# Performance work log

Hardware: AMD Instinct MI355X
Metric: run time of the kernel (lower is better)

## Reference

```python
import jax, jax.numpy as jnp
import numpy as np

N = 100000      # nodes
E = 1600000     # edges
F_IN = 512      # num_node_features
HID = 128       # hidden_dim (GCN2Conv channels)
C = 64          # num_classes
L = 8           # n_layers
ALPHA = 0.1
THETA = 0.5


def setup_inputs() -> dict:
    key = jax.random.key(0)
    ks = jax.random.split(key, 7)
    x = jax.random.normal(ks[0], (N, F_IN), jnp.float32)
    edge_index = jax.random.randint(ks[1], (2, E), 0, N, dtype=jnp.int64)
    # fcs[0]: Linear(F_IN, HID); stored as [in, out] so forward is x @ w + b
    w_in = jax.random.normal(ks[2], (F_IN, HID), jnp.float32) / np.sqrt(F_IN)
    b_in = jnp.zeros((HID,), jnp.float32)
    # one shared [H, H] weight per GCN2Conv layer (shared_weights=True)
    conv_w = jax.random.normal(ks[3], (L, HID, HID), jnp.float32) / np.sqrt(HID)
    # fcs[-1]: Linear(HID, C)
    w_out = jax.random.normal(ks[4], (HID, C), jnp.float32) / np.sqrt(HID)
    b_out = jnp.zeros((C,), jnp.float32)
    return dict(x=x, edge_index=edge_index, w_in=w_in, b_in=b_in,
                conv_w=conv_w, w_out=w_out, b_out=b_out)


def _gcn_norm(edge_index, num_nodes):
    # PyG gcn_norm with add_self_loops=True, edge_weight=1
    loops = jnp.arange(num_nodes, dtype=edge_index.dtype)
    src = jnp.concatenate([edge_index[0], loops])
    dst = jnp.concatenate([edge_index[1], loops])
    deg = jax.ops.segment_sum(jnp.ones_like(dst, jnp.float32), dst,
                              num_segments=num_nodes)
    dinv = jnp.where(deg > 0, jax.lax.rsqrt(jnp.maximum(deg, 1e-12)), 0.0)
    norm = dinv[src] * dinv[dst]  # [E + N]
    return src, dst, norm


def reference(x, edge_index, w_in, b_in, conv_w, w_out, b_out):
    src, dst, norm = _gcn_norm(edge_index, N)
    h = x @ w_in + b_in          # fcs[0]; [N, HID]
    h0 = h                       # initial residual
    for l in range(L):
        beta = float(np.log(THETA / (l + 1) + 1.0))
        # sparse neighbor aggregation: out[i] = sum_e norm[e] * h[src[e]]
        agg = jax.ops.segment_sum(h[src] * norm[:, None], dst, num_segments=N)
        s = (1.0 - ALPHA) * agg + ALPHA * h0           # initial residual mix
        h = jax.nn.elu((1.0 - beta) * s + beta * (s @ conv_w[l]))  # identity mapping
        # dropout omitted (eval mode / training=False)
    logits = h @ w_out + b_out   # fcs[-1]
    return jax.nn.log_softmax(logits, axis=-1)
```

## Files before the change

kernel.cpp:

```cpp
#include <hip/hip_runtime.h>
#include <math.h>

#define N_NODES 100000
#define N_EDGES 1600000
#define F_IN    512
#define HID     128
#define NCLS    64
#define NLAYERS 8
#define NT      (N_NODES / 16)
#define NSCANB  ((N_NODES + 255) / 256)

typedef __attribute__((ext_vector_type(8))) short short8;
typedef __attribute__((ext_vector_type(4))) float float4v;

__device__ inline unsigned short f2bf(float f) {
    unsigned int u = __float_as_uint(f);
    unsigned int r = u + 0x7fffu + ((u >> 16) & 1u);
    return (unsigned short)(r >> 16);
}
__device__ inline float bf2f(unsigned short h) {
    return __uint_as_float(((unsigned int)h) << 16);
}
__device__ inline uint4 pack8(const unsigned short* v) {
    uint4 u;
    u.x = (unsigned)v[0] | ((unsigned)v[1] << 16);
    u.y = (unsigned)v[2] | ((unsigned)v[3] << 16);
    u.z = (unsigned)v[4] | ((unsigned)v[5] << 16);
    u.w = (unsigned)v[6] | ((unsigned)v[7] << 16);
    return u;
}
__device__ inline void bf8_fma(float* a, uint4 u, float v) {
    a[0] += v * __uint_as_float(u.x << 16);
    a[1] += v * __uint_as_float(u.x & 0xffff0000u);
    a[2] += v * __uint_as_float(u.y << 16);
    a[3] += v * __uint_as_float(u.y & 0xffff0000u);
    a[4] += v * __uint_as_float(u.z << 16);
    a[5] += v * __uint_as_float(u.z & 0xffff0000u);
    a[6] += v * __uint_as_float(u.w << 16);
    a[7] += v * __uint_as_float(u.w & 0xffff0000u);
}
__device__ inline void split_into(short8& ahi, short8& alo, int j, float f) {
    unsigned short h = f2bf(f);
    ahi[j] = (short)h;
    alo[j] = (short)f2bf(f - bf2f(h));
}


__global__ __launch_bounds__(256) void cnt_init(int* __restrict__ cnt) {
    int i = blockIdx.x * 256 + threadIdx.x;
    if (i < N_NODES) cnt[i] = 0;
}
__global__ __launch_bounds__(256) void cnt_count(const int* __restrict__ dst,
                                                 int* __restrict__ cnt) {
    int e = blockIdx.x * 256 + threadIdx.x;
    if (e < N_EDGES) atomicAdd(&cnt[dst[e]], 1);
}
__global__ __launch_bounds__(256) void make_dinv(const int* __restrict__ cnt,
                                                 float* __restrict__ dinv) {
    int i = blockIdx.x * 256 + threadIdx.x;
    if (i < N_NODES) dinv[i] = rsqrtf((float)(cnt[i] + 1));
}
__global__ __launch_bounds__(256) void scan_block(const int* __restrict__ cnt,
                                                  int* __restrict__ partial,
                                                  int* __restrict__ bsum) {
    __shared__ int tmp[256];
    int t = threadIdx.x, i = blockIdx.x * 256 + t;
    int v = (i < N_NODES) ? cnt[i] : 0;
    tmp[t] = v;
    __syncthreads();
#pragma unroll
    for (int off = 1; off < 256; off <<= 1) {
        int add = (t >= off) ? tmp[t - off] : 0;
        __syncthreads();
        tmp[t] += add;
        __syncthreads();
    }
    if (i < N_NODES) partial[i] = tmp[t];
    if (t == 255) bsum[blockIdx.x] = tmp[255];
}
__global__ void scan_bsum(int* __restrict__ bsum) {
    if (threadIdx.x == 0 && blockIdx.x == 0) {
        int acc = 0;
        for (int i = 0; i < NSCANB; i++) { int v = bsum[i]; bsum[i] = acc; acc += v; }
    }
}
__global__ __launch_bounds__(256) void finalize_rowptr(const int* __restrict__ cnt,
                                                       const int* __restrict__ partial,
                                                       const int* __restrict__ bsum,
                                                       int* __restrict__ row_ptr,
                                                       int* __restrict__ cursor) {
    int i = blockIdx.x * 256 + threadIdx.x;
    if (i < N_NODES) {
        int ex = partial[i] - cnt[i] + bsum[blockIdx.x];
        row_ptr[i] = ex;
        cursor[i]  = ex;
        if (i == N_NODES - 1) row_ptr[N_NODES] = ex + cnt[i];
    }
}
__global__ __launch_bounds__(256) void scatter_edges(const int* __restrict__ srcI,
                                                     const int* __restrict__ dstI,
                                                     const float* __restrict__ dinv,
                                                     int* __restrict__ cursor,
                                                     int2* __restrict__ rec) {
    int e = blockIdx.x * 256 + threadIdx.x;
    if (e < N_EDGES) {
        int s = srcI[e], d = dstI[e];
        int pos = atomicAdd(&cursor[d], 1);
        rec[pos] = make_int2(s, __float_as_int(dinv[s] * dinv[d]));
    }
}

__global__ __launch_bounds__(64) void conv_win(const float* __restrict__ w,
                                               unsigned short* __restrict__ wip) {
    int nt = blockIdx.x >> 4;
    int c  = blockIdx.x & 15;
    int lane = threadIdx.x;
    int n  = nt * 16 + (lane & 15);
    int kb = c * 32 + (lane >> 4) * 8;
    unsigned short hi[8], lo[8];
#pragma unroll
    for (int j = 0; j < 8; j++) {
        float v = w[(size_t)(kb + j) * HID + n];
        hi[j] = f2bf(v);
        lo[j] = f2bf(v - bf2f(hi[j]));
    }
    size_t base = ((size_t)c * 8 + nt) * 1024 + (size_t)lane * 8;
    *(uint4*)&wip[base]       = pack8(hi);
    *(uint4*)&wip[base + 512] = pack8(lo);
}

__global__ __launch_bounds__(64) void conv_wl(const float* __restrict__ cw,
                                              unsigned short* __restrict__ wlp) {
    int l  = blockIdx.x >> 5;
    int nt = (blockIdx.x >> 2) & 7;
    int c  = blockIdx.x & 3;
    int lane = threadIdx.x;
    float beta = logf(0.5f / (float)(l + 1) + 1.0f);
    int n  = nt * 16 + (lane & 15);
    int kb = c * 32 + (lane >> 4) * 8;
    const float* W = cw + (size_t)l * HID * HID;
    unsigned short hi[8], lo[8];
#pragma unroll
    for (int j = 0; j < 8; j++) {
        int k = kb + j;
        float v = beta * W[(size_t)k * HID + n] + ((k == n) ? (1.0f - beta) : 0.0f);
        hi[j] = f2bf(v);
        lo[j] = f2bf(v - bf2f(hi[j]));
    }
    size_t base = (size_t)l * 32768 + ((size_t)c * 8 + nt) * 1024 + (size_t)lane * 8;
    *(uint4*)&wlp[base]       = pack8(hi);
    *(uint4*)&wlp[base + 512] = pack8(lo);
}

__global__ __launch_bounds__(64) void conv_wout(const float* __restrict__ w,
                                                unsigned short* __restrict__ wop) {
    int nt = blockIdx.x >> 2;
    int c  = blockIdx.x & 3;
    int lane = threadIdx.x;
    int n  = nt * 16 + (lane & 15);
    int kb = c * 32 + (lane >> 4) * 8;
    unsigned short hi[8], lo[8];
#pragma unroll
    for (int j = 0; j < 8; j++) {
        float v = w[(size_t)(kb + j) * NCLS + n];
        hi[j] = f2bf(v);
        lo[j] = f2bf(v - bf2f(hi[j]));
    }
    size_t base = ((size_t)nt * 4 + c) * 1024 + (size_t)lane * 8;
    *(uint4*)&wop[base]       = pack8(hi);
    *(uint4*)&wop[base + 512] = pack8(lo);
}

__global__ __launch_bounds__(256) void in_gemm_mfma(const float* __restrict__ x,
        const unsigned short* __restrict__ wip, const float* __restrict__ bias,
        unsigned short* __restrict__ hb, unsigned short* __restrict__ h0b) {
    __shared__ unsigned short wlds[8192];
    __shared__ unsigned short tile[64][136];
    int tid = threadIdx.x;
    int wave = tid >> 6, lane = tid & 63;
    int t = blockIdx.x * 4 + wave;
    int m = lane & 15, q = lane >> 4;
    int tc = (t < NT) ? t : (NT - 1);

    const uint4* wg = (const uint4*)wip;
    uint4 pf0 = wg[tid];
    uint4 pf1 = wg[tid + 256];
    uint4 pf2 = wg[tid + 512];
    uint4 pf3 = wg[tid + 768];

    float4v acc[8];
#pragma unroll
    for (int nt = 0; nt < 8; nt++) acc[nt] = (float4v){0.f, 0.f, 0.f, 0.f};
    const float* xr = x + (size_t)(tc * 16 + m) * F_IN + q * 8;
    uint4* wl4 = (uint4*)wlds;

    for (int c = 0; c < 16; c++) {
        wl4[tid] = pf0; wl4[tid + 256] = pf1; wl4[tid + 512] = pf2; wl4[tid + 768] = pf3;
        __syncthreads();
        if (c < 15) {
            const uint4* wn = wg + (size_t)(c + 1) * 1024;
            pf0 = wn[tid]; pf1 = wn[tid + 256]; pf2 = wn[tid + 512]; pf3 = wn[tid + 768];
        }
        float4 x0 = *(const float4*)(xr + c * 32);
        float4 x1 = *(const float4*)(xr + c * 32 + 4);
        short8 ahi, alo;
        split_into(ahi, alo, 0, x0.x); split_into(ahi, alo, 1, x0.y);
        split_into(ahi, alo, 2, x0.z); split_into(ahi, alo, 3, x0.w);
        split_into(ahi, alo, 4, x1.x); split_into(ahi, alo, 5, x1.y);
        split_into(ahi, alo, 6, x1.z); split_into(ahi, alo, 7, x1.w);
#pragma unroll
        for (int nt = 0; nt < 8; nt++) {
            short8 bhi = *(short8*)&wlds[nt * 1024 + lane * 8];
            short8 blo = *(short8*)&wlds[nt * 1024 + 512 + lane * 8];
            acc[nt] = __builtin_amdgcn_mfma_f32_16x16x32_bf16(ahi, bhi, acc[nt], 0, 0, 0);
            acc[nt] = __builtin_amdgcn_mfma_f32_16x16x32_bf16(ahi, blo, acc[nt], 0, 0, 0);
            acc[nt] = __builtin_amdgcn_mfma_f32_16x16x32_bf16(alo, bhi, acc[nt], 0, 0, 0);
        }
        __syncthreads();
    }

    if (t < NT) {
#pragma unroll
        for (int nt = 0; nt < 8; nt++) {
            float bb = bias[nt * 16 + m];
#pragma unroll
            for (int r = 0; r < 4; r++)
                tile[wave * 16 + q * 4 + r][nt * 16 + m] = f2bf(acc[nt][r] + bb);
        }
    }
    __syncthreads();

    int nl = tid >> 2, part = tid & 3;
    int node = blockIdx.x * 64 + nl;
    if (node < N_NODES) {
        uint4* d1 = (uint4*)&hb [(size_t)node * HID + part * 32];
        uint4* d2 = (uint4*)&h0b[(size_t)node * HID + part * 32];
#pragma unroll
        for (int j = 0; j < 4; j++) {
            uint4 u = *(uint4*)&tile[nl][part * 32 + j * 8];
            d1[j] = u; d2[j] = u;
        }
    }
}

__global__ __launch_bounds__(256) void spmm_mix(const int* __restrict__ row_ptr,
        const int2* __restrict__ rec, const float* __restrict__ dinv,
        const unsigned short* __restrict__ hb, const unsigned short* __restrict__ h0b,
        float* __restrict__ sout) {
    int node = blockIdx.x * 4 + (threadIdx.x >> 6);
    int lane = threadIdx.x & 63;
    int quarter = lane >> 4;
    int fl = lane & 15;
    int e0 = row_ptr[node], e1 = row_ptr[node + 1];
    float a[8] = {0.f, 0.f, 0.f, 0.f, 0.f, 0.f, 0.f, 0.f};

    int e = e0 + quarter;
    for (; e + 12 < e1; e += 16) {
        int2 r0 = rec[e];
        int2 r1 = rec[e + 4];
        int2 r2 = rec[e + 8];
        int2 r3 = rec[e + 12];
        uint4 u0 = *(const uint4*)(hb + (size_t)r0.x * HID + fl * 8);
        uint4 u1 = *(const uint4*)(hb + (size_t)r1.x * HID + fl * 8);
        uint4 u2 = *(const uint4*)(hb + (size_t)r2.x * HID + fl * 8);
        uint4 u3 = *(const uint4*)(hb + (size_t)r3.x * HID + fl * 8);
        bf8_fma(a, u0, __int_as_float(r0.y));
        bf8_fma(a, u1, __int_as_float(r1.y));
        bf8_fma(a, u2, __int_as_float(r2.y));
        bf8_fma(a, u3, __int_as_float(r3.y));
    }
    for (; e + 4 < e1; e += 8) {
        int2 r0 = rec[e];
        int2 r1 = rec[e + 4];
        uint4 u0 = *(const uint4*)(hb + (size_t)r0.x * HID + fl * 8);
        uint4 u1 = *(const uint4*)(hb + (size_t)r1.x * HID + fl * 8);
        bf8_fma(a, u0, __int_as_float(r0.y));
        bf8_fma(a, u1, __int_as_float(r1.y));
    }
    for (; e < e1; e += 4) {
        int2 r0 = rec[e];
        uint4 u0 = *(const uint4*)(hb + (size_t)r0.x * HID + fl * 8);
        bf8_fma(a, u0, __int_as_float(r0.y));
    }
#pragma unroll
    for (int j = 0; j < 8; j++) {
        a[j] += __shfl_xor(a[j], 16);
        a[j] += __shfl_xor(a[j], 32);
    }
    if (quarter == 0) {
        float dd = dinv[node], d2 = dd * dd;
        uint4 hv = *(const uint4*)(hb  + (size_t)node * HID + fl * 8);
        uint4 zv = *(const uint4*)(h0b + (size_t)node * HID + fl * 8);
        float hvf[8], zvf[8];
        hvf[0] = __uint_as_float(hv.x << 16); hvf[1] = __uint_as_float(hv.x & 0xffff0000u);
        hvf[2] = __uint_as_float(hv.y << 16); hvf[3] = __uint_as_float(hv.y & 0xffff0000u);
        hvf[4] = __uint_as_float(hv.z << 16); hvf[5] = __uint_as_float(hv.z & 0xffff0000u);
        hvf[6] = __uint_as_float(hv.w << 16); hvf[7] = __uint_as_float(hv.w & 0xffff0000u);
        zvf[0] = __uint_as_float(zv.x << 16); zvf[1] = __uint_as_float(zv.x & 0xffff0000u);
        zvf[2] = __uint_as_float(zv.y << 16); zvf[3] = __uint_as_float(zv.y & 0xffff0000u);
        zvf[4] = __uint_as_float(zv.z << 16); zvf[5] = __uint_as_float(zv.z & 0xffff0000u);
        zvf[6] = __uint_as_float(zv.w << 16); zvf[7] = __uint_as_float(zv.w & 0xffff0000u);
        float o[8];
#pragma unroll
        for (int j = 0; j < 8; j++)
            o[j] = 0.9f * (a[j] + d2 * hvf[j]) + 0.1f * zvf[j];
        float4* dst = (float4*)(sout + (size_t)node * HID + fl * 8);
        dst[0] = make_float4(o[0], o[1], o[2], o[3]);
        dst[1] = make_float4(o[4], o[5], o[6], o[7]);
    }
}

__global__ __launch_bounds__(256) void layer_gemm_bf(const float* __restrict__ s,
        const unsigned short* __restrict__ wlp, unsigned short* __restrict__ hb) {
    __shared__ unsigned short wlds[8192];
    __shared__ unsigned short tile[64][136];
    int tid = threadIdx.x;
    int wave = tid >> 6, lane = tid & 63;
    int t = blockIdx.x * 4 + wave;
    int m = lane & 15, q = lane >> 4;
    int tc = (t < NT) ? t : (NT - 1);

    const uint4* wg = (const uint4*)wlp;
    uint4 pf0 = wg[tid];
    uint4 pf1 = wg[tid + 256];
    uint4 pf2 = wg[tid + 512];
    uint4 pf3 = wg[tid + 768];

    float4v acc[8];
#pragma unroll
    for (int nt = 0; nt < 8; nt++) acc[nt] = (float4v){0.f, 0.f, 0.f, 0.f};
    const float* sr = s + (size_t)(tc * 16 + m) * HID + q * 8;
    uint4* wl4 = (uint4*)wlds;

#pragma unroll
    for (int c = 0; c < 4; c++) {
        wl4[tid] = pf0; wl4[tid + 256] = pf1; wl4[tid + 512] = pf2; wl4[tid + 768] = pf3;
        __syncthreads();
        if (c < 3) {
            const uint4* wn = wg + (size_t)(c + 1) * 1024;
            pf0 = wn[tid]; pf1 = wn[tid + 256]; pf2 = wn[tid + 512]; pf3 = wn[tid + 768];
        }
        float4 x0 = *(const float4*)(sr + c * 32);
        float4 x1 = *(const float4*)(sr + c * 32 + 4);
        short8 ahi, alo;
        split_into(ahi, alo, 0, x0.x); split_into(ahi, alo, 1, x0.y);
        split_into(ahi, alo, 2, x0.z); split_into(ahi, alo, 3, x0.w);
        split_into(ahi, alo, 4, x1.x); split_into(ahi, alo, 5, x1.y);
        split_into(ahi, alo, 6, x1.z); split_into(ahi, alo, 7, x1.w);
#pragma unroll
        for (int nt = 0; nt < 8; nt++) {
            short8 bhi = *(short8*)&wlds[nt * 1024 + lane * 8];
            short8 blo = *(short8*)&wlds[nt * 1024 + 512 + lane * 8];
            acc[nt] = __builtin_amdgcn_mfma_f32_16x16x32_bf16(ahi, bhi, acc[nt], 0, 0, 0);
            acc[nt] = __builtin_amdgcn_mfma_f32_16x16x32_bf16(ahi, blo, acc[nt], 0, 0, 0);
            acc[nt] = __builtin_amdgcn_mfma_f32_16x16x32_bf16(alo, bhi, acc[nt], 0, 0, 0);
        }
        __syncthreads();
    }

    if (t < NT) {
#pragma unroll
        for (int nt = 0; nt < 8; nt++) {
#pragma unroll
            for (int r = 0; r < 4; r++) {
                float v = acc[nt][r];
                v = (v > 0.f) ? v : (expf(v) - 1.0f);
                tile[wave * 16 + q * 4 + r][nt * 16 + m] = f2bf(v);
            }
        }
    }
    __syncthreads();

    int nl = tid >> 2, part = tid & 3;
    int node = blockIdx.x * 64 + nl;
    if (node < N_NODES) {
        uint4* d1 = (uint4*)&hb[(size_t)node * HID + part * 32];
#pragma unroll
        for (int j = 0; j < 4; j++) d1[j] = *(uint4*)&tile[nl][part * 32 + j * 8];
    }
}

__global__ __launch_bounds__(256) void layer_gemm_last(const float* __restrict__ s,
        const unsigned short* __restrict__ wlp, float* __restrict__ hf) {
    int wave = threadIdx.x >> 6;
    int lane = threadIdx.x & 63;
    int t = blockIdx.x * 4 + wave;
    int m = lane & 15, q = lane >> 4;
    if (t >= NT) return;

    float4v acc[8];
#pragma unroll
    for (int nt = 0; nt < 8; nt++) acc[nt] = (float4v){0.f, 0.f, 0.f, 0.f};
    const float* sr = s + (size_t)(t * 16 + m) * HID + q * 8;
    const short8* wp8 = (const short8*)wlp;
#pragma unroll
    for (int c = 0; c < 4; c++) {
        float4 x0 = *(const float4*)(sr + c * 32);
        float4 x1 = *(const float4*)(sr + c * 32 + 4);
        short8 ahi, alo;
        split_into(ahi, alo, 0, x0.x); split_into(ahi, alo, 1, x0.y);
        split_into(ahi, alo, 2, x0.z); split_into(ahi, alo, 3, x0.w);
        split_into(ahi, alo, 4, x1.x); split_into(ahi, alo, 5, x1.y);
        split_into(ahi, alo, 6, x1.z); split_into(ahi, alo, 7, x1.w);
#pragma unroll
        for (int nt = 0; nt < 8; nt++) {
            short8 bhi = wp8[(size_t)(c * 8 + nt) * 128 + lane];
            short8 blo = wp8[(size_t)(c * 8 + nt) * 128 + 64 + lane];
            acc[nt] = __builtin_amdgcn_mfma_f32_16x16x32_bf16(ahi, bhi, acc[nt], 0, 0, 0);
            acc[nt] = __builtin_amdgcn_mfma_f32_16x16x32_bf16(ahi, blo, acc[nt], 0, 0, 0);
            acc[nt] = __builtin_amdgcn_mfma_f32_16x16x32_bf16(alo, bhi, acc[nt], 0, 0, 0);
        }
    }
#pragma unroll
    for (int nt = 0; nt < 8; nt++) {
#pragma unroll
        for (int r = 0; r < 4; r++) {
            float v = acc[nt][r];
            v = (v > 0.f) ? v : (expf(v) - 1.0f);
            hf[(size_t)(t * 16 + q * 4 + r) * HID + nt * 16 + m] = v;
        }
    }
}

__global__ __launch_bounds__(256) void out_gemm(const float* __restrict__ hf,
        const unsigned short* __restrict__ wop, const float* __restrict__ bias,
        float* __restrict__ out) {
    int wave = threadIdx.x >> 6;
    int lane = threadIdx.x & 63;
    int t = blockIdx.x * 4 + wave;
    int m = lane & 15, q = lane >> 4;
    if (t >= NT) return;

    float4v acc[4];
#pragma unroll
    for (int nt = 0; nt < 4; nt++) acc[nt] = (float4v){0.f, 0.f, 0.f, 0.f};
    const float* hr = hf + (size_t)(t * 16 + m) * HID + q * 8;
    const short8* wp8 = (const short8*)wop;
#pragma unroll
    for (int c = 0; c < 4; c++) {
        float4 x0 = *(const float4*)(hr + c * 32);
        float4 x1 = *(const float4*)(hr + c * 32 + 4);
        short8 ahi, alo;
        split_into(ahi, alo, 0, x0.x); split_into(ahi, alo, 1, x0.y);
        split_into(ahi, alo, 2, x0.z); split_into(ahi, alo, 3, x0.w);
        split_into(ahi, alo, 4, x1.x); split_into(ahi, alo, 5, x1.y);
        split_into(ahi, alo, 6, x1.z); split_into(ahi, alo, 7, x1.w);
#pragma unroll
        for (int nt = 0; nt < 4; nt++) {
            short8 bhi = wp8[(size_t)(nt * 4 + c) * 128 + lane];
            short8 blo = wp8[(size_t)(nt * 4 + c) * 128 + 64 + lane];
            acc[nt] = __builtin_amdgcn_mfma_f32_16x16x32_bf16(ahi, bhi, acc[nt], 0, 0, 0);
            acc[nt] = __builtin_amdgcn_mfma_f32_16x16x32_bf16(ahi, blo, acc[nt], 0, 0, 0);
            acc[nt] = __builtin_amdgcn_mfma_f32_16x16x32_bf16(alo, bhi, acc[nt], 0, 0, 0);
        }
    }
    float bn[4];
#pragma unroll
    for (int nt = 0; nt < 4; nt++) bn[nt] = bias[nt * 16 + m];
#pragma unroll
    for (int r = 0; r < 4; r++) {
        float v0 = acc[0][r] + bn[0], v1 = acc[1][r] + bn[1];
        float v2 = acc[2][r] + bn[2], v3 = acc[3][r] + bn[3];
        float mx = fmaxf(fmaxf(v0, v1), fmaxf(v2, v3));
#pragma unroll
        for (int msk = 1; msk < 16; msk <<= 1) mx = fmaxf(mx, __shfl_xor(mx, msk));
        float ssum = expf(v0 - mx) + expf(v1 - mx) + expf(v2 - mx) + expf(v3 - mx);
#pragma unroll
        for (int msk = 1; msk < 16; msk <<= 1) ssum += __shfl_xor(ssum, msk);
        float lg = mx + logf(ssum);
        size_t base = (size_t)(t * 16 + q * 4 + r) * NCLS + m;
        out[base]      = v0 - lg;
        out[base + 16] = v1 - lg;
        out[base + 32] = v2 - lg;
        out[base + 48] = v3 - lg;
    }
}


extern "C" void kernel_launch(void* const* d_in, const int* in_sizes, int n_in,
                              void* d_out, int out_size, void* d_ws, size_t ws_size,
                              hipStream_t stream) {
    const float* x      = (const float*)d_in[0];
    const int*   ei     = (const int*)  d_in[1];
    const float* w_in   = (const float*)d_in[2];
    const float* b_in   = (const float*)d_in[3];
    const float* conv_w = (const float*)d_in[4];
    const float* w_out  = (const float*)d_in[5];
    const float* b_out  = (const float*)d_in[6];
    float* out = (float*)d_out;

    const int* srcI = ei;
    const int* dstI = ei + N_EDGES;

    char* ws = (char*)d_ws;
    float* dinv    = (float*)(ws + 0x000000);
    int*   cnt     = (int*)  (ws + 0x080000);
    int*   partial = (int*)  (ws + 0x100000);
    int*   bsum    = (int*)  (ws + 0x180000);
    int*   row_ptr = (int*)  (ws + 0x190000);
    int*   cursor  = (int*)  (ws + 0x200000);
    int2*  rec     = (int2*) (ws + 0x280000);
    unsigned short* wip = (unsigned short*)(ws + 0xF00000);
    unsigned short* wlp = (unsigned short*)(ws + 0xF40000);
    unsigned short* wop = (unsigned short*)(ws + 0xFC0000);
    unsigned short* hb  = (unsigned short*)(ws + 0x1000000);
    unsigned short* h0b = hb + (size_t)N_NODES * HID;
    float* sbuf = (float*)(h0b + (size_t)N_NODES * HID);
    float* hf   = sbuf + (size_t)N_NODES * HID;

    int gN = (N_NODES + 255) / 256;
    int gE = (N_EDGES + 255) / 256;
    int gT = (NT + 3) / 4;

    cnt_init<<<gN, 256, 0, stream>>>(cnt);
    cnt_count<<<gE, 256, 0, stream>>>(dstI, cnt);
    make_dinv<<<gN, 256, 0, stream>>>(cnt, dinv);
    scan_block<<<NSCANB, 256, 0, stream>>>(cnt, partial, bsum);
    scan_bsum<<<1, 64, 0, stream>>>(bsum);
    finalize_rowptr<<<NSCANB, 256, 0, stream>>>(cnt, partial, bsum, row_ptr, cursor);
    scatter_edges<<<gE, 256, 0, stream>>>(srcI, dstI, dinv, cursor, rec);

    conv_win<<<128, 64, 0, stream>>>(w_in, wip);
    conv_wl<<<256, 64, 0, stream>>>(conv_w, wlp);
    conv_wout<<<16, 64, 0, stream>>>(w_out, wop);

    in_gemm_mfma<<<gT, 256, 0, stream>>>(x, wip, b_in, hb, h0b);

    for (int l = 0; l < NLAYERS; l++) {
        spmm_mix<<<N_NODES / 4, 256, 0, stream>>>(row_ptr, rec, dinv, hb, h0b, sbuf);
        const unsigned short* wl = wlp + (size_t)l * 32768;
        if (l < NLAYERS - 1)
            layer_gemm_bf<<<gT, 256, 0, stream>>>(sbuf, wl, hb);
        else
            layer_gemm_last<<<gT, 256, 0, stream>>>(sbuf, wl, hf);
    }

    out_gemm<<<gT, 256, 0, stream>>>(hf, wop, b_out, out);
}
```

Before: 1.270 ms.

## Fuse SpMM aggregation with per-layer GEMM via LDS-staged bf16 fragments

Merges the sparse neighbor aggregation and the layer GEMM into one kernel per layer. Aggregated rows are split into bf16 hi/lo and written to swizzled shared memory as MFMA A-fragments, so the fp32 intermediate no longer makes a round trip through global memory. The hidden state now ping-pongs between two buffers, and each 16-lane group handles one node with sequential edges instead of splitting edges across quarters. This removes a launch and traffic per layer, but it changes the gather parallelism and latency hiding for skewed degrees and raises LDS use per block.

Result: faster. 1.218 ms (-4.0%).

```diff
diff --git a/kernel.cpp b/kernel.cpp
--- a/kernel.cpp
+++ b/kernel.cpp
@@ -12,6 +12,8 @@
 
 typedef __attribute__((ext_vector_type(8))) short short8;
 typedef __attribute__((ext_vector_type(4))) float float4v;
+
+#define SWZB(b) ((b) ^ ((((b) >> 8) & 3) << 4))
 
 __device__ inline unsigned short f2bf(float f) {
     unsigned int u = __float_as_uint(f);
@@ -38,6 +40,12 @@
     a[5] += v * __uint_as_float(u.z & 0xffff0000u);
     a[6] += v * __uint_as_float(u.w << 16);
     a[7] += v * __uint_as_float(u.w & 0xffff0000u);
+}
+__device__ inline void unpack8(float* f, uint4 u) {
+    f[0] = __uint_as_float(u.x << 16); f[1] = __uint_as_float(u.x & 0xffff0000u);
+    f[2] = __uint_as_float(u.y << 16); f[3] = __uint_as_float(u.y & 0xffff0000u);
+    f[4] = __uint_as_float(u.z << 16); f[5] = __uint_as_float(u.z & 0xffff0000u);
+    f[6] = __uint_as_float(u.w << 16); f[7] = __uint_as_float(u.w & 0xffff0000u);
 }
 __device__ inline void split_into(short8& ahi, short8& alo, int j, float f) {
     unsigned short h = f2bf(f);
@@ -243,167 +251,69 @@
     }
 }
 
-__global__ __launch_bounds__(256) void spmm_mix(const int* __restrict__ row_ptr,
+template <int LAST>
+__global__ __launch_bounds__(256, 4) void spmm_gemm(const int* __restrict__ row_ptr,
         const int2* __restrict__ rec, const float* __restrict__ dinv,
-        const unsigned short* __restrict__ hb, const unsigned short* __restrict__ h0b,
-        float* __restrict__ sout) {
-    int node = blockIdx.x * 4 + (threadIdx.x >> 6);
-    int lane = threadIdx.x & 63;
-    int quarter = lane >> 4;
-    int fl = lane & 15;
-    int e0 = row_ptr[node], e1 = row_ptr[node + 1];
-    float a[8] = {0.f, 0.f, 0.f, 0.f, 0.f, 0.f, 0.f, 0.f};
-
-    int e = e0 + quarter;
-    for (; e + 12 < e1; e += 16) {
-        int2 r0 = rec[e];
-        int2 r1 = rec[e + 4];
-        int2 r2 = rec[e + 8];
-        int2 r3 = rec[e + 12];
-        uint4 u0 = *(const uint4*)(hb + (size_t)r0.x * HID + fl * 8);
-        uint4 u1 = *(const uint4*)(hb + (size_t)r1.x * HID + fl * 8);
-        uint4 u2 = *(const uint4*)(hb + (size_t)r2.x * HID + fl * 8);
-        uint4 u3 = *(const uint4*)(hb + (size_t)r3.x * HID + fl * 8);
-        bf8_fma(a, u0, __int_as_float(r0.y));
-        bf8_fma(a, u1, __int_as_float(r1.y));
-        bf8_fma(a, u2, __int_as_float(r2.y));
-        bf8_fma(a, u3, __int_as_float(r3.y));
-    }
-    for (; e + 4 < e1; e += 8) {
-        int2 r0 = rec[e];
-        int2 r1 = rec[e + 4];
-        uint4 u0 = *(const uint4*)(hb + (size_t)r0.x * HID + fl * 8);
-        uint4 u1 = *(const uint4*)(hb + (size_t)r1.x * HID + fl * 8);
-        bf8_fma(a, u0, __int_as_float(r0.y));
-        bf8_fma(a, u1, __int_as_float(r1.y));
-    }
-    for (; e < e1; e += 4) {
-        int2 r0 = rec[e];
-        uint4 u0 = *(const uint4*)(hb + (size_t)r0.x * HID + fl * 8);
-        bf8_fma(a, u0, __int_as_float(r0.y));
-    }
-#pragma unroll
-    for (int j = 0; j < 8; j++) {
-        a[j] += __shfl_xor(a[j], 16);
-        a[j] += __shfl_xor(a[j], 32);
-    }
-    if (quarter == 0) {
-        float dd = dinv[node], d2 = dd * dd;
-        uint4 hv = *(const uint4*)(hb  + (size_t)node * HID + fl * 8);
-        uint4 zv = *(const uint4*)(h0b + (size_t)node * HID + fl * 8);
-        float hvf[8], zvf[8];
-        hvf[0] = __uint_as_float(hv.x << 16); hvf[1] = __uint_as_float(hv.x & 0xffff0000u);
-        hvf[2] = __uint_as_float(hv.y << 16); hvf[3] = __uint_as_float(hv.y & 0xffff0000u);
-        hvf[4] = __uint_as_float(hv.z << 16); hvf[5] = __uint_as_float(hv.z & 0xffff0000u);
-        hvf[6] = __uint_as_float(hv.w << 16); hvf[7] = __uint_as_float(hv.w & 0xffff0000u);
-        zvf[0] = __uint_as_float(zv.x << 16); zvf[1] = __uint_as_float(zv.x & 0xffff0000u);
-        zvf[2] = __uint_as_float(zv.y << 16); zvf[3] = __uint_as_float(zv.y & 0xffff0000u);
-        zvf[4] = __uint_as_float(zv.z << 16); zvf[5] = __uint_as_float(zv.z & 0xffff0000u);
-        zvf[6] = __uint_as_float(zv.w << 16); zvf[7] = __uint_as_float(zv.w & 0xffff0000u);
-        float o[8];
-#pragma unroll
-        for (int j = 0; j < 8; j++)
-            o[j] = 0.9f * (a[j] + d2 * hvf[j]) + 0.1f * zvf[j];
-        float4* dst = (float4*)(sout + (size_t)node * HID + fl * 8);
-        dst[0] = make_float4(o[0], o[1], o[2], o[3]);
-        dst[1] = make_float4(o[4], o[5], o[6], o[7]);
-    }
-}
-
-__global__ __launch_bounds__(256) void layer_gemm_bf(const float* __restrict__ s,
-        const unsigned short* __restrict__ wlp, unsigned short* __restrict__ hb) {
-    __shared__ unsigned short wlds[8192];
-    __shared__ unsigned short tile[64][136];
+        const unsigned short* __restrict__ hin, const unsigned short* __restrict__ h0b,
+        const unsigned short* __restrict__ wlp, void* __restrict__ outp) {
+    __shared__ __align__(16) unsigned short afr[16384];
     int tid = threadIdx.x;
     int wave = tid >> 6, lane = tid & 63;
-    int t = blockIdx.x * 4 + wave;
-    int m = lane & 15, q = lane >> 4;
-    int tc = (t < NT) ? t : (NT - 1);
-
-    const uint4* wg = (const uint4*)wlp;
-    uint4 pf0 = wg[tid];
-    uint4 pf1 = wg[tid + 256];
-    uint4 pf2 = wg[tid + 512];
-    uint4 pf3 = wg[tid + 768];
+    int qu = lane >> 4, fl = lane & 15;
+    char* af = (char*)afr;
+
+    int base = blockIdx.x * 64 + wave * 16;
+#pragma unroll 1
+    for (int g = 0; g < 4; ++g) {
+        int node = base + g * 4 + qu;
+        int nc = (node < N_NODES) ? node : (N_NODES - 1);
+        int e0 = row_ptr[nc], e1 = row_ptr[nc + 1];
+        float a[8] = {0.f, 0.f, 0.f, 0.f, 0.f, 0.f, 0.f, 0.f};
+        int e = e0;
+        for (; e + 3 < e1; e += 4) {
+            int2 r0 = rec[e], r1 = rec[e + 1], r2 = rec[e + 2], r3 = rec[e + 3];
+            uint4 u0 = *(const uint4*)(hin + (size_t)r0.x * HID + fl * 8);
+            uint4 u1 = *(const uint4*)(hin + (size_t)r1.x * HID + fl * 8);
+            uint4 u2 = *(const uint4*)(hin + (size_t)r2.x * HID + fl * 8);
+            uint4 u3 = *(const uint4*)(hin + (size_t)r3.x * HID + fl * 8);
+            bf8_fma(a, u0, __int_as_float(r0.y));
+            bf8_fma(a, u1, __int_as_float(r1.y));
+            bf8_fma(a, u2, __int_as_float(r2.y));
+            bf8_fma(a, u3, __int_as_float(r3.y));
+        }
+        for (; e < e1; ++e) {
+            int2 r0 = rec[e];
+            uint4 u0 = *(const uint4*)(hin + (size_t)r0.x * HID + fl * 8);
+            bf8_fma(a, u0, __int_as_float(r0.y));
+        }
+        float dd = dinv[nc], d2 = dd * dd;
+        float hvf[8], zvf[8];
+        unpack8(hvf, *(const uint4*)(hin + (size_t)nc * HID + fl * 8));
+        unpack8(zvf, *(const uint4*)(h0b + (size_t)nc * HID + fl * 8));
+        short8 ohi, olo;
+#pragma unroll
+        for (int j = 0; j < 8; ++j) {
+            float o = 0.9f * (a[j] + d2 * hvf[j]) + 0.1f * zvf[j];
+            split_into(ohi, olo, j, o);
+        }
+        int mrow = g * 4 + qu;
+        int b0 = wave * 8192 + (fl >> 2) * 2048 + (fl & 3) * 256 + mrow * 16;
+        *(short8*)(af + SWZB(b0)) = ohi;
+        *(short8*)(af + SWZB(b0 + 1024)) = olo;
+    }
+    __syncthreads();
 
     float4v acc[8];
 #pragma unroll
-    for (int nt = 0; nt < 8; nt++) acc[nt] = (float4v){0.f, 0.f, 0.f, 0.f};
-    const float* sr = s + (size_t)(tc * 16 + m) * HID + q * 8;
-    uint4* wl4 = (uint4*)wlds;
-
-#pragma unroll
-    for (int c = 0; c < 4; c++) {
-        wl4[tid] = pf0; wl4[tid + 256] = pf1; wl4[tid + 512] = pf2; wl4[tid + 768] = pf3;
-        __syncthreads();
-        if (c < 3) {
-            const uint4* wn = wg + (size_t)(c + 1) * 1024;
-            pf0 = wn[tid]; pf1 = wn[tid + 256]; pf2 = wn[tid + 512]; pf3 = wn[tid + 768];
-        }
-        float4 x0 = *(const float4*)(sr + c * 32);
-        float4 x1 = *(const float4*)(sr + c * 32 + 4);
-        short8 ahi, alo;
-        split_into(ahi, alo, 0, x0.x); split_into(ahi, alo, 1, x0.y);
-        split_into(ahi, alo, 2, x0.z); split_into(ahi, alo, 3, x0.w);
-        split_into(ahi, alo, 4, x1.x); split_into(ahi, alo, 5, x1.y);
-        split_into(ahi, alo, 6, x1.z); split_into(ahi, alo, 7, x1.w);
-#pragma unroll
-        for (int nt = 0; nt < 8; nt++) {
-            short8 bhi = *(short8*)&wlds[nt * 1024 + lane * 8];
-            short8 blo = *(short8*)&wlds[nt * 1024 + 512 + lane * 8];
-            acc[nt] = __builtin_amdgcn_mfma_f32_16x16x32_bf16(ahi, bhi, acc[nt], 0, 0, 0);
-            acc[nt] = __builtin_amdgcn_mfma_f32_16x16x32_bf16(ahi, blo, acc[nt], 0, 0, 0);
-            acc[nt] = __builtin_amdgcn_mfma_f32_16x16x32_bf16(alo, bhi, acc[nt], 0, 0, 0);
-        }
-        __syncthreads();
-    }
-
-    if (t < NT) {
-#pragma unroll
-        for (int nt = 0; nt < 8; nt++) {
-#pragma unroll
-            for (int r = 0; r < 4; r++) {
-                float v = acc[nt][r];
-                v = (v > 0.f) ? v : (expf(v) - 1.0f);
-                tile[wave * 16 + q * 4 + r][nt * 16 + m] = f2bf(v);
-            }
-        }
-    }
-    __syncthreads();
-
-    int nl = tid >> 2, part = tid & 3;
-    int node = blockIdx.x * 64 + nl;
-    if (node < N_NODES) {
-        uint4* d1 = (uint4*)&hb[(size_t)node * HID + part * 32];
-#pragma unroll
-        for (int j = 0; j < 4; j++) d1[j] = *(uint4*)&tile[nl][part * 32 + j * 8];
-    }
-}
-
-__global__ __launch_bounds__(256) void layer_gemm_last(const float* __restrict__ s,
-        const unsigned short* __restrict__ wlp, float* __restrict__ hf) {
-    int wave = threadIdx.x >> 6;
-    int lane = threadIdx.x & 63;
-    int t = blockIdx.x * 4 + wave;
-    int m = lane & 15, q = lane >> 4;
-    if (t >= NT) return;
-
-    float4v acc[8];
-#pragma unroll
-    for (int nt = 0; nt < 8; nt++) acc[nt] = (float4v){0.f, 0.f, 0.f, 0.f};
-    const float* sr = s + (size_t)(t * 16 + m) * HID + q * 8;
+    for (int nt = 0; nt < 8; ++nt) acc[nt] = (float4v){0.f, 0.f, 0.f, 0.f};
     const short8* wp8 = (const short8*)wlp;
 #pragma unroll
-    for (int c = 0; c < 4; c++) {
-        float4 x0 = *(const float4*)(sr + c * 32);
-        float4 x1 = *(const float4*)(sr + c * 32 + 4);
-        short8 ahi, alo;
-        split_into(ahi, alo, 0, x0.x); split_into(ahi, alo, 1, x0.y);
-        split_into(ahi, alo, 2, x0.z); split_into(ahi, alo, 3, x0.w);
-        split_into(ahi, alo, 4, x1.x); split_into(ahi, alo, 5, x1.y);
-        split_into(ahi, alo, 6, x1.z); split_into(ahi, alo, 7, x1.w);
-#pragma unroll
-        for (int nt = 0; nt < 8; nt++) {
+    for (int c = 0; c < 4; ++c) {
+        int rb = wave * 8192 + c * 2048 + lane * 16;
+        short8 ahi = *(const short8*)(af + SWZB(rb));
+        short8 alo = *(const short8*)(af + SWZB(rb + 1024));
+#pragma unroll
+        for (int nt = 0; nt < 8; ++nt) {
             short8 bhi = wp8[(size_t)(c * 8 + nt) * 128 + lane];
             short8 blo = wp8[(size_t)(c * 8 + nt) * 128 + 64 + lane];
             acc[nt] = __builtin_amdgcn_mfma_f32_16x16x32_bf16(ahi, bhi, acc[nt], 0, 0, 0);
@@ -411,13 +321,41 @@
             acc[nt] = __builtin_amdgcn_mfma_f32_16x16x32_bf16(alo, bhi, acc[nt], 0, 0, 0);
         }
     }
-#pragma unroll
-    for (int nt = 0; nt < 8; nt++) {
-#pragma unroll
-        for (int r = 0; r < 4; r++) {
-            float v = acc[nt][r];
-            v = (v > 0.f) ? v : (expf(v) - 1.0f);
-            hf[(size_t)(t * 16 + q * 4 + r) * HID + nt * 16 + m] = v;
+
+    if (LAST) {
+        int t = blockIdx.x * 4 + wave;
+        if (t < NT) {
+            float* hf = (float*)outp;
+#pragma unroll
+            for (int nt = 0; nt < 8; ++nt) {
+#pragma unroll
+                for (int r = 0; r < 4; ++r) {
+                    float v = acc[nt][r];
+                    v = (v > 0.f) ? v : (expf(v) - 1.0f);
+                    hf[(size_t)(t * 16 + qu * 4 + r) * HID + nt * 16 + fl] = v;
+                }
+            }
+        }
+    } else {
+        __syncthreads();
+        unsigned short (*tile)[136] = (unsigned short (*)[136])afr;
+#pragma unroll
+        for (int nt = 0; nt < 8; ++nt) {
+#pragma unroll
+            for (int r = 0; r < 4; ++r) {
+                float v = acc[nt][r];
+                v = (v > 0.f) ? v : (expf(v) - 1.0f);
+                tile[wave * 16 + qu * 4 + r][nt * 16 + fl] = f2bf(v);
+            }
+        }
+        __syncthreads();
+        unsigned short* hout = (unsigned short*)outp;
+        int nl = tid >> 2, part = tid & 3;
+        int node = blockIdx.x * 64 + nl;
+        if (node < N_NODES) {
+            uint4* d1 = (uint4*)&hout[(size_t)node * HID + part * 32];
+#pragma unroll
+            for (int j = 0; j < 4; ++j) d1[j] = *(uint4*)&tile[nl][part * 32 + j * 8];
         }
     }
 }
@@ -505,8 +443,8 @@
     unsigned short* wop = (unsigned short*)(ws + 0xFC0000);
     unsigned short* hb  = (unsigned short*)(ws + 0x1000000);
     unsigned short* h0b = hb + (size_t)N_NODES * HID;
-    float* sbuf = (float*)(h0b + (size_t)N_NODES * HID);
-    float* hf   = sbuf + (size_t)N_NODES * HID;
+    unsigned short* hb2 = h0b + (size_t)N_NODES * HID;
+    float* hf = (float*)(hb2 + 2 * (size_t)N_NODES * HID);
 
     int gN = (N_NODES + 255) / 256;
     int gE = (N_EDGES + 255) / 256;
@@ -526,13 +464,16 @@
 
     in_gemm_mfma<<<gT, 256, 0, stream>>>(x, wip, b_in, hb, h0b);
 
+    unsigned short* cur = hb;
+    unsigned short* nxt = hb2;
     for (int l = 0; l < NLAYERS; l++) {
-        spmm_mix<<<N_NODES / 4, 256, 0, stream>>>(row_ptr, rec, dinv, hb, h0b, sbuf);
         const unsigned short* wl = wlp + (size_t)l * 32768;
-        if (l < NLAYERS - 1)
-            layer_gemm_bf<<<gT, 256, 0, stream>>>(sbuf, wl, hb);
-        else
-            layer_gemm_last<<<gT, 256, 0, stream>>>(sbuf, wl, hf);
+        if (l < NLAYERS - 1) {
+            spmm_gemm<0><<<gT, 256, 0, stream>>>(row_ptr, rec, dinv, cur, h0b, wl, nxt);
+            unsigned short* t = cur; cur = nxt; nxt = t;
+        } else {
+            spmm_gemm<1><<<gT, 256, 0, stream>>>(row_ptr, rec, dinv, cur, h0b, wl, hf);
+        }
     }
 
     out_gemm<<<gT, 256, 0, stream>>>(hf, wop, b_out, out);
```
